# Kernel tuning notes

Measured on AMD Instinct MI355X. Metric: run time of the kernel, lower is better.

Reference implementation:

```python
import jax, jax.numpy as jnp
import numpy as np


def setup_inputs() -> dict:
    key = jax.random.key(0)
    k1, k2, k3, k4 = jax.random.split(key, 4)
    dim, b, q_len, c_len = 1024, 16, 1024, 2048
    q = jax.random.normal(k1, (q_len, b, dim), dtype=jnp.float32)
    c = jax.random.normal(k2, (c_len, b, dim), dtype=jnp.float32)
    # torch nn.Linear weights: [out_features, in_features]
    W_in = jax.random.normal(k3, (dim, dim), dtype=jnp.float32) * (dim ** -0.5)
    W_out = jax.random.normal(k4, (dim, 2 * dim), dtype=jnp.float32) * ((2 * dim) ** -0.5)
    return {"q": q, "c": c, "W_in": W_in, "W_out": W_out}


def reference(q, c, W_in, W_out):
    # q: [q_len, b, dim] -> [b, q_len, dim]; c: [c_len, b, dim] -> [b, c_len, dim]
    qb = jnp.transpose(q, (1, 0, 2))
    cb = jnp.transpose(c, (1, 0, 2))
    qb = jnp.einsum('bqd,ed->bqe', qb, W_in)            # linear_in (no bias)
    score = jnp.einsum('bqd,bkd->bqk', qb, cb)          # unscaled QK^T
    score = jax.nn.softmax(score, axis=-1)              # [b, q_len, c_len]
    ctx = jnp.einsum('bqk,bkd->bqd', score, cb)         # score @ c
    cat = jnp.concatenate([ctx, qb], axis=-1)           # [b, q_len, 2*dim]
    out = jnp.tanh(jnp.einsum('bqf,df->bqd', cat, W_out))
    return (jnp.transpose(out, (1, 0, 2)), score)       # ([q_len,b,dim], [b,q_len,c_len])
```

## Files before the change

kernel.cpp:

```cpp
#include <hip/hip_runtime.h>
#include <hip/hip_bf16.h>
#include <stdint.h>


typedef __bf16 bf16x8 __attribute__((ext_vector_type(8)));
typedef float floatx4 __attribute__((ext_vector_type(4)));

__device__ __forceinline__ unsigned short f2bf_rne(float f) {
  unsigned int u = __float_as_uint(f);
  u += 0x7FFFu + ((u >> 16) & 1u);
  return (unsigned short)(u >> 16);
}
__device__ __forceinline__ float bf2f(unsigned short h) {
  return __uint_as_float(((unsigned int)h) << 16);
}

__device__ __forceinline__ void async_load16(const void* g, void* l) {
  __builtin_amdgcn_global_load_lds(
      (const __attribute__((address_space(1))) void*)g,
      (__attribute__((address_space(3))) void*)l,
      16, 0, 0);
}

__global__ __launch_bounds__(256) void split_kernel(
    const float* __restrict__ x, unsigned short* __restrict__ hi,
    unsigned short* __restrict__ lo, long n4)
{
  long i = (long)blockIdx.x * 256 + threadIdx.x;
  if (i >= n4) return;
  float4 v = ((const float4*)x)[i];
  ushort4 h;
  h.x = f2bf_rne(v.x); h.y = f2bf_rne(v.y);
  h.z = f2bf_rne(v.z); h.w = f2bf_rne(v.w);
  ((ushort4*)hi)[i] = h;
  if (lo) {
    ushort4 l;
    l.x = f2bf_rne(v.x - bf2f(h.x));
    l.y = f2bf_rne(v.y - bf2f(h.y));
    l.z = f2bf_rne(v.z - bf2f(h.z));
    l.w = f2bf_rne(v.w - bf2f(h.w));
    ((ushort4*)lo)[i] = l;
  }
}

__global__ __launch_bounds__(256) void transpose_kernel(
    const float* __restrict__ c, unsigned short* __restrict__ ct)
{
  __shared__ unsigned short t[64 * 68];
  int k0 = blockIdx.x * 64;
  int d0 = blockIdx.y * 64;
  int b  = blockIdx.z;
  int tid = threadIdx.x;
  #pragma unroll
  for (int p4 = 0; p4 < 4; ++p4) {
    int idx = p4 * 256 + tid;
    int kr = idx >> 4;
    int dc = (idx & 15) * 4;
    float4 v = *(const float4*)&c[(long)(k0 + kr) * 16384 + (long)b * 1024 + d0 + dc];
    ushort4 h;
    h.x = f2bf_rne(v.x); h.y = f2bf_rne(v.y);
    h.z = f2bf_rne(v.z); h.w = f2bf_rne(v.w);
    *(ushort4*)&t[kr * 68 + dc] = h;
  }
  __syncthreads();
  #pragma unroll
  for (int p4 = 0; p4 < 4; ++p4) {
    int idx = p4 * 256 + tid;
    int dr = idx >> 4;
    int kc = (idx & 15) * 4;
    ushort4 o;
    o.x = t[(kc + 0) * 68 + dr];
    o.y = t[(kc + 1) * 68 + dr];
    o.z = t[(kc + 2) * 68 + dr];
    o.w = t[(kc + 3) * 68 + dr];
    *(ushort4*)&ct[(long)b * 2097152 + (long)(d0 + dr) * 2048 + k0 + kc] = o;
  }
}

__global__ __launch_bounds__(256) void softmax_kernel(
    float* __restrict__ S, unsigned short* __restrict__ P)
{
  __shared__ float sred[8];
  long row = blockIdx.x;
  float* p = S + row * 2048;
  int tid = threadIdx.x;
  int lane = tid & 63, w = tid >> 6;
  float4 v0 = ((float4*)p)[tid];
  float4 v1 = ((float4*)p)[tid + 256];
  float m = fmaxf(fmaxf(fmaxf(v0.x, v0.y), fmaxf(v0.z, v0.w)),
                  fmaxf(fmaxf(v1.x, v1.y), fmaxf(v1.z, v1.w)));
  #pragma unroll
  for (int off = 32; off; off >>= 1) m = fmaxf(m, __shfl_xor(m, off));
  if (lane == 0) sred[w] = m;
  __syncthreads();
  m = fmaxf(fmaxf(sred[0], sred[1]), fmaxf(sred[2], sred[3]));
  v0.x = __expf(v0.x - m); v0.y = __expf(v0.y - m);
  v0.z = __expf(v0.z - m); v0.w = __expf(v0.w - m);
  v1.x = __expf(v1.x - m); v1.y = __expf(v1.y - m);
  v1.z = __expf(v1.z - m); v1.w = __expf(v1.w - m);
  float s = v0.x + v0.y + v0.z + v0.w + v1.x + v1.y + v1.z + v1.w;
  #pragma unroll
  for (int off = 32; off; off >>= 1) s += __shfl_xor(s, off);
  if (lane == 0) sred[4 + w] = s;
  __syncthreads();
  s = sred[4] + sred[5] + sred[6] + sred[7];
  float inv = 1.0f / s;
  v0.x *= inv; v0.y *= inv; v0.z *= inv; v0.w *= inv;
  v1.x *= inv; v1.y *= inv; v1.z *= inv; v1.w *= inv;
  ((float4*)p)[tid] = v0;
  ((float4*)p)[tid + 256] = v1;
  unsigned short* pp = P + row * 2048;
  ushort4 b0, b1;
  b0.x = f2bf_rne(v0.x); b0.y = f2bf_rne(v0.y);
  b0.z = f2bf_rne(v0.z); b0.w = f2bf_rne(v0.w);
  b1.x = f2bf_rne(v1.x); b1.y = f2bf_rne(v1.y);
  b1.z = f2bf_rne(v1.z); b1.w = f2bf_rne(v1.w);
  ((ushort4*)pp)[tid] = b0;
  ((ushort4*)pp)[tid + 256] = b1;
}

template<int SPLIT, int MODE>
__global__ __launch_bounds__(256, 2) void gemm_kernel(
    const unsigned short* __restrict__ Ah, const unsigned short* __restrict__ Al,
    long sAb, long ldA,
    const unsigned short* __restrict__ Bh, const unsigned short* __restrict__ Bl,
    long sBb, long ldB,
    void* __restrict__ Cp, long sCb, long ldC,
    unsigned short* __restrict__ P1, unsigned short* __restrict__ P2,
    int K, int SM, int SN, int GM)
{
  constexpr int BK  = SPLIT ? 32 : 64;
  constexpr int KB8 = BK / 8;
  constexpr int ISS = (128 * KB8) / 256;
  constexpr int NT  = SPLIT ? 4 : 2;
  __shared__ unsigned short lds[16384];

  const int tid  = threadIdx.x;
  const int lane = tid & 63;
  const int w    = tid >> 6;
  const int wm   = w >> 1;
  const int wn   = w & 1;
  const int bz   = blockIdx.z;

  const int flat = blockIdx.x + gridDim.x * blockIdx.y;
  const int sub  = flat & 7;
  const int g    = flat >> 3;
  const long mt  = (long)(sub % GM) * SM + (g / SN);
  const long nt  = (long)(sub / GM) * SN + (g % SN);
  const long m0  = mt * 128;
  const long n0  = nt * 128;

  const unsigned short* a0 = Ah + bz * sAb + m0 * ldA;
  const unsigned short* a1 = SPLIT ? (Al + bz * sAb + m0 * ldA) : a0;
  const unsigned short* b0 = Bh + bz * sBb + n0 * ldB;
  const unsigned short* b1 = SPLIT ? (Bl + bz * sBb + n0 * ldB) : b0;

  floatx4 acc[4][4] = {};

  for (int kt = 0; kt < K; kt += BK) {
    #pragma unroll
    for (int t = 0; t < NT; ++t) {
      const unsigned short* src;
      long ld;
      int base;
      if (SPLIT) {
        src  = (t == 0) ? a0 : (t == 1) ? a1 : (t == 2) ? b0 : b1;
        ld   = (t < 2) ? ldA : ldB;
        base = t * 4096;
      } else {
        src  = (t == 0) ? a0 : b0;
        ld   = (t == 0) ? ldA : ldB;
        base = t * 8192;
      }
      #pragma unroll
      for (int it = 0; it < ISS; ++it) {
        int s   = it * 256 + tid;
        int row = s / KB8;
        int kb  = (s & (KB8 - 1)) ^ (SPLIT ? ((row >> 1) & 3) : (row & 7));
        const unsigned short* g2 = src + (long)row * ld + kt + kb * 8;
        async_load16(g2, &lds[base + (it * 256 + w * 64) * 8]);
      }
    }
    __syncthreads();

    #pragma unroll
    for (int kk = 0; kk < BK / 32; ++kk) {
      bf16x8 fbh[4], fbl[4];
      #pragma unroll
      for (int j = 0; j < 4; ++j) {
        int r    = wn * 64 + j * 16 + (lane & 15);
        int kb   = (lane >> 4) + kk * 4;
        int slot = r * KB8 + (kb ^ (SPLIT ? ((r >> 1) & 3) : (r & 7)));
        fbh[j] = *(const bf16x8*)&lds[8192 + slot * 8];
        if (SPLIT) fbl[j] = *(const bf16x8*)&lds[12288 + slot * 8];
      }
      #pragma unroll
      for (int i = 0; i < 4; ++i) {
        int r    = wm * 64 + i * 16 + (lane & 15);
        int kb   = (lane >> 4) + kk * 4;
        int slot = r * KB8 + (kb ^ (SPLIT ? ((r >> 1) & 3) : (r & 7)));
        bf16x8 fah = *(const bf16x8*)&lds[slot * 8];
        bf16x8 fal = fah;
        if (SPLIT) fal = *(const bf16x8*)&lds[4096 + slot * 8];
        #pragma unroll
        for (int j = 0; j < 4; ++j) {
          acc[i][j] = __builtin_amdgcn_mfma_f32_16x16x32_bf16(fah, fbh[j], acc[i][j], 0, 0, 0);
          if (SPLIT) {
            acc[i][j] = __builtin_amdgcn_mfma_f32_16x16x32_bf16(fah, fbl[j], acc[i][j], 0, 0, 0);
            acc[i][j] = __builtin_amdgcn_mfma_f32_16x16x32_bf16(fal, fbh[j], acc[i][j], 0, 0, 0);
          }
        }
      }
    }
    __syncthreads();
  }

  #pragma unroll
  for (int i = 0; i < 4; ++i) {
    #pragma unroll
    for (int j = 0; j < 4; ++j) {
      #pragma unroll
      for (int t = 0; t < 4; ++t) {
        long rg = m0 + wm * 64 + i * 16 + (lane >> 4) * 4 + t;
        long cg = n0 + wn * 64 + j * 16 + (lane & 15);
        float v = acc[i][j][t];
        if (MODE == 0) {
          ((float*)Cp)[bz * sCb + rg * ldC + cg] = v;
        } else if (MODE == 1) {
          ((unsigned short*)Cp)[bz * sCb + rg * ldC + cg] = f2bf_rne(v);
        } else if (MODE == 2) {
          long qq = rg & 1023, bb = rg >> 10;
          ((float*)Cp)[(qq * 16 + bb) * 1024 + cg] = tanhf(v);
        } else {
          unsigned short hv = f2bf_rne(v);
          unsigned short lv = f2bf_rne(v - bf2f(hv));
          P1[rg * 1024 + cg] = hv;
          P2[rg * 1024 + cg] = lv;
          long bb = rg & 15, qq = rg >> 4;
          ((unsigned short*)Cp)[(bb * 1024 + qq) * 2048 + 1024 + cg] = hv;
        }
      }
    }
  }
}

extern "C" void kernel_launch(void* const* d_in, const int* in_sizes, int n_in,
                              void* d_out, int out_size, void* d_ws, size_t ws_size,
                              hipStream_t stream)
{
  const float* q    = (const float*)d_in[0];
  const float* c    = (const float*)d_in[1];
  const float* Win  = (const float*)d_in[2];
  const float* Wout = (const float*)d_in[3];

  char* ws = (char*)d_ws;
  const size_t MB = 1024u * 1024u;

  unsigned short* qh  = (unsigned short*)(ws);
  unsigned short* ch  = (unsigned short*)(ws);
  unsigned short* pb  = (unsigned short*)(ws);
  unsigned short* qbh = (unsigned short*)(ws + 64 * MB);
  unsigned short* qbl = (unsigned short*)(ws + 96 * MB);
  unsigned short* ct  = (unsigned short*)(ws + 64 * MB);
  unsigned short* cat = (unsigned short*)(ws + 128 * MB);
  unsigned short* Wh  = (unsigned short*)(ws + 192 * MB);
  unsigned short* Wl  = (unsigned short*)(ws + 194 * MB);
  unsigned short* Wo  = (unsigned short*)(ws + 196 * MB);

  unsigned short* ql  = (unsigned short*)d_out;
  unsigned short* cl  = (unsigned short*)d_out;
  float* out0  = (float*)d_out;
  float* score = (float*)d_out + 16777216;

  split_kernel<<<16384, 256, 0, stream>>>(q,    qh, ql,      4194304L);
  split_kernel<<<1024,  256, 0, stream>>>(Win,  Wh, Wl,      262144L);
  split_kernel<<<2048,  256, 0, stream>>>(Wout, Wo, nullptr, 524288L);

  gemm_kernel<1, 3><<<dim3(128, 8, 1), 256, 0, stream>>>(
      qh, ql, 0L, 1024L, Wh, Wl, 0L, 1024L,
      (void*)cat, 0L, 0L, qbh, qbl, 1024, 32, 4, 4);

  split_kernel<<<32768, 256, 0, stream>>>(c, ch, cl, 8388608L);

  gemm_kernel<1, 0><<<dim3(8, 16, 16), 256, 0, stream>>>(
      qbh, qbl, 1024L, 16384L, ch, cl, 1024L, 16384L,
      (void*)score, 2097152L, 2048L, nullptr, nullptr, 1024, 4, 4, 2);

  transpose_kernel<<<dim3(32, 16, 16), 256, 0, stream>>>(c, ct);
  softmax_kernel<<<16384, 256, 0, stream>>>(score, pb);

  gemm_kernel<0, 1><<<dim3(8, 8, 16), 256, 0, stream>>>(
      pb, nullptr, 2097152L, 2048L, ct, nullptr, 2097152L, 2048L,
      (void*)cat, 2097152L, 2048L, nullptr, nullptr, 2048, 4, 2, 2);

  gemm_kernel<0, 2><<<dim3(128, 8, 1), 256, 0, stream>>>(
      cat, nullptr, 0L, 2048L, Wo, nullptr, 0L, 2048L,
      (void*)out0, 0L, 0L, nullptr, nullptr, 2048, 32, 4, 4);

  (void)in_sizes; (void)n_in; (void)out_size; (void)ws_size;
}
```

Baseline: 964.9 us.

## Rewrite GEMM as 256x256 tile, 512-thread kernel with 4-stage async LDS pipeline

The GEMM kernel moves from 128x128 tiles with 256 threads and a synchronous load-then-compute loop to 256x256 tiles with 512 threads (8 waves, 128x64 per wave). It uses a 4-slot LDS ring buffer with three stages prefetched, explicit vmcnt waits and a single barrier per step. The split-precision (hi/lo) products become three separate virtual k-steps, each issuing one MFMA per fragment pair, and MFMA sections get raised wave priority. This is meant to hide global-to-LDS latency and raise data reuse per loaded byte. In exchange it uses 128KB of LDS and more accumulator registers, which may limit occupancy, and the grids become coarser with fewer blocks per GEMM.

```diff
diff --git a/kernel.cpp b/kernel.cpp
--- a/kernel.cpp
+++ b/kernel.cpp
@@ -120,7 +120,7 @@
 }
 
 template<int SPLIT, int MODE>
-__global__ __launch_bounds__(256, 2) void gemm_kernel(
+__global__ __launch_bounds__(512, 2) void gemm_kernel(
     const unsigned short* __restrict__ Ah, const unsigned short* __restrict__ Al,
     long sAb, long ldA,
     const unsigned short* __restrict__ Bh, const unsigned short* __restrict__ Bl,
@@ -129,17 +129,13 @@
     unsigned short* __restrict__ P1, unsigned short* __restrict__ P2,
     int K, int SM, int SN, int GM)
 {
-  constexpr int BK  = SPLIT ? 32 : 64;
-  constexpr int KB8 = BK / 8;
-  constexpr int ISS = (128 * KB8) / 256;
-  constexpr int NT  = SPLIT ? 4 : 2;
-  __shared__ unsigned short lds[16384];
+  __shared__ __align__(16) unsigned short lds[65536];
 
   const int tid  = threadIdx.x;
   const int lane = tid & 63;
   const int w    = tid >> 6;
-  const int wm   = w >> 1;
-  const int wn   = w & 1;
+  const int wm   = w >> 2;
+  const int wn   = w & 3;
   const int bz   = blockIdx.z;
 
   const int flat = blockIdx.x + gridDim.x * blockIdx.y;
@@ -147,81 +143,92 @@
   const int g    = flat >> 3;
   const long mt  = (long)(sub % GM) * SM + (g / SN);
   const long nt  = (long)(sub / GM) * SN + (g % SN);
-  const long m0  = mt * 128;
-  const long n0  = nt * 128;
+  const long m0  = mt * 256;
+  const long n0  = nt * 256;
 
   const unsigned short* a0 = Ah + bz * sAb + m0 * ldA;
   const unsigned short* a1 = SPLIT ? (Al + bz * sAb + m0 * ldA) : a0;
   const unsigned short* b0 = Bh + bz * sBb + n0 * ldB;
   const unsigned short* b1 = SPLIT ? (Bl + bz * sBb + n0 * ldB) : b0;
 
-  floatx4 acc[4][4] = {};
-
-  for (int kt = 0; kt < K; kt += BK) {
+  const int s0r = tid >> 2,        s1r = (512 + tid) >> 2;
+  const int s0k = (tid & 3) ^ ((s0r >> 1) & 3);
+  const int s1k = ((512 + tid) & 3) ^ ((s1r >> 1) & 3);
+  const long offA0 = (long)s0r * ldA + s0k * 8;
+  const long offA1 = (long)s1r * ldA + s1k * 8;
+  const long offB0 = (long)s0r * ldB + s0k * 8;
+  const long offB1 = (long)s1r * ldB + s1k * 8;
+  const int d0 = w * 512;
+  const int d1 = 4096 + w * 512;
+
+  const int nkt = SPLIT ? 3 * (K / 32) : (K / 32);
+
+  floatx4 acc[8][4] = {};
+
+  auto stage = [&](int vt2) {
+    const int slot = vt2 & 3;
+    const unsigned short* As;
+    const unsigned short* Bs;
+    long ks;
+    if (SPLIT) {
+      int term = vt2 % 3;
+      ks = (long)(vt2 / 3) * 32;
+      As = (term < 2) ? a0 : a1;
+      Bs = (term == 1) ? b1 : b0;
+    } else {
+      As = a0; Bs = b0; ks = (long)vt2 * 32;
+    }
+    const int ab = slot * 8192;
+    const int bb = 32768 + slot * 8192;
+    async_load16(As + offA0 + ks, &lds[ab + d0]);
+    async_load16(As + offA1 + ks, &lds[ab + d1]);
+    async_load16(Bs + offB0 + ks, &lds[bb + d0]);
+    async_load16(Bs + offB1 + ks, &lds[bb + d1]);
+  };
+
+  stage(0); stage(1); stage(2);
+
+  for (int vt = 0; vt < nkt; ++vt) {
+    const int ahead = nkt - 1 - vt;
+    if (ahead >= 2)      asm volatile("s_waitcnt vmcnt(8)" ::: "memory");
+    else if (ahead == 1) asm volatile("s_waitcnt vmcnt(4)" ::: "memory");
+    else                 asm volatile("s_waitcnt vmcnt(0)" ::: "memory");
+    __builtin_amdgcn_s_barrier();
+    __builtin_amdgcn_sched_barrier(0);
+
+    if (vt + 3 < nkt) stage(vt + 3);
+    __builtin_amdgcn_sched_barrier(0);
+
+    const unsigned short* At = &lds[(vt & 3) * 8192];
+    const unsigned short* Bt = &lds[32768 + (vt & 3) * 8192];
+
+    bf16x8 fb[4];
     #pragma unroll
-    for (int t = 0; t < NT; ++t) {
-      const unsigned short* src;
-      long ld;
-      int base;
-      if (SPLIT) {
-        src  = (t == 0) ? a0 : (t == 1) ? a1 : (t == 2) ? b0 : b1;
-        ld   = (t < 2) ? ldA : ldB;
-        base = t * 4096;
-      } else {
-        src  = (t == 0) ? a0 : b0;
-        ld   = (t == 0) ? ldA : ldB;
-        base = t * 8192;
-      }
+    for (int j = 0; j < 4; ++j) {
+      int r    = wn * 64 + j * 16 + (lane & 15);
+      int slot = r * 4 + ((lane >> 4) ^ ((r >> 1) & 3));
+      fb[j] = *(const bf16x8*)&Bt[slot * 8];
+    }
+    __builtin_amdgcn_s_setprio(1);
+    #pragma unroll
+    for (int i = 0; i < 8; ++i) {
+      int r    = wm * 128 + i * 16 + (lane & 15);
+      int slot = r * 4 + ((lane >> 4) ^ ((r >> 1) & 3));
+      bf16x8 fa = *(const bf16x8*)&At[slot * 8];
       #pragma unroll
-      for (int it = 0; it < ISS; ++it) {
-        int s   = it * 256 + tid;
-        int row = s / KB8;
-        int kb  = (s & (KB8 - 1)) ^ (SPLIT ? ((row >> 1) & 3) : (row & 7));
-        const unsigned short* g2 = src + (long)row * ld + kt + kb * 8;
-        async_load16(g2, &lds[base + (it * 256 + w * 64) * 8]);
-      }
+      for (int j = 0; j < 4; ++j)
+        acc[i][j] = __builtin_amdgcn_mfma_f32_16x16x32_bf16(fa, fb[j], acc[i][j], 0, 0, 0);
     }
-    __syncthreads();
-
-    #pragma unroll
-    for (int kk = 0; kk < BK / 32; ++kk) {
-      bf16x8 fbh[4], fbl[4];
-      #pragma unroll
-      for (int j = 0; j < 4; ++j) {
-        int r    = wn * 64 + j * 16 + (lane & 15);
-        int kb   = (lane >> 4) + kk * 4;
-        int slot = r * KB8 + (kb ^ (SPLIT ? ((r >> 1) & 3) : (r & 7)));
-        fbh[j] = *(const bf16x8*)&lds[8192 + slot * 8];
-        if (SPLIT) fbl[j] = *(const bf16x8*)&lds[12288 + slot * 8];
-      }
-      #pragma unroll
-      for (int i = 0; i < 4; ++i) {
-        int r    = wm * 64 + i * 16 + (lane & 15);
-        int kb   = (lane >> 4) + kk * 4;
-        int slot = r * KB8 + (kb ^ (SPLIT ? ((r >> 1) & 3) : (r & 7)));
-        bf16x8 fah = *(const bf16x8*)&lds[slot * 8];
-        bf16x8 fal = fah;
-        if (SPLIT) fal = *(const bf16x8*)&lds[4096 + slot * 8];
-        #pragma unroll
-        for (int j = 0; j < 4; ++j) {
-          acc[i][j] = __builtin_amdgcn_mfma_f32_16x16x32_bf16(fah, fbh[j], acc[i][j], 0, 0, 0);
-          if (SPLIT) {
-            acc[i][j] = __builtin_amdgcn_mfma_f32_16x16x32_bf16(fah, fbl[j], acc[i][j], 0, 0, 0);
-            acc[i][j] = __builtin_amdgcn_mfma_f32_16x16x32_bf16(fal, fbh[j], acc[i][j], 0, 0, 0);
-          }
-        }
-      }
-    }
-    __syncthreads();
-  }
-
-  #pragma unroll
-  for (int i = 0; i < 4; ++i) {
+    __builtin_amdgcn_s_setprio(0);
+  }
+
+  #pragma unroll
+  for (int i = 0; i < 8; ++i) {
     #pragma unroll
     for (int j = 0; j < 4; ++j) {
       #pragma unroll
       for (int t = 0; t < 4; ++t) {
-        long rg = m0 + wm * 64 + i * 16 + (lane >> 4) * 4 + t;
+        long rg = m0 + wm * 128 + i * 16 + (lane >> 4) * 4 + t;
         long cg = n0 + wn * 64 + j * 16 + (lane & 15);
         float v = acc[i][j][t];
         if (MODE == 0) {
@@ -276,26 +283,26 @@
   split_kernel<<<1024,  256, 0, stream>>>(Win,  Wh, Wl,      262144L);
   split_kernel<<<2048,  256, 0, stream>>>(Wout, Wo, nullptr, 524288L);
 
-  gemm_kernel<1, 3><<<dim3(128, 8, 1), 256, 0, stream>>>(
+  gemm_kernel<1, 3><<<dim3(32, 8, 1), 512, 0, stream>>>(
       qh, ql, 0L, 1024L, Wh, Wl, 0L, 1024L,
-      (void*)cat, 0L, 0L, qbh, qbl, 1024, 32, 4, 4);
+      (void*)cat, 0L, 0L, qbh, qbl, 1024, 8, 4, 8);
 
   split_kernel<<<32768, 256, 0, stream>>>(c, ch, cl, 8388608L);
 
-  gemm_kernel<1, 0><<<dim3(8, 16, 16), 256, 0, stream>>>(
+  gemm_kernel<1, 0><<<dim3(4, 8, 16), 512, 0, stream>>>(
       qbh, qbl, 1024L, 16384L, ch, cl, 1024L, 16384L,
-      (void*)score, 2097152L, 2048L, nullptr, nullptr, 1024, 4, 4, 2);
+      (void*)score, 2097152L, 2048L, nullptr, nullptr, 1024, 2, 2, 2);
 
   transpose_kernel<<<dim3(32, 16, 16), 256, 0, stream>>>(c, ct);
   softmax_kernel<<<16384, 256, 0, stream>>>(score, pb);
 
-  gemm_kernel<0, 1><<<dim3(8, 8, 16), 256, 0, stream>>>(
+  gemm_kernel<0, 1><<<dim3(4, 4, 16), 512, 0, stream>>>(
       pb, nullptr, 2097152L, 2048L, ct, nullptr, 2097152L, 2048L,
-      (void*)cat, 2097152L, 2048L, nullptr, nullptr, 2048, 4, 2, 2);
-
-  gemm_kernel<0, 2><<<dim3(128, 8, 1), 256, 0, stream>>>(
+      (void*)cat, 2097152L, 2048L, nullptr, nullptr, 2048, 1, 2, 4);
+
+  gemm_kernel<0, 2><<<dim3(32, 8, 1), 512, 0, stream>>>(
       cat, nullptr, 0L, 2048L, Wo, nullptr, 0L, 2048L,
-      (void*)out0, 0L, 0L, nullptr, nullptr, 2048, 32, 4, 4);
+      (void*)out0, 0L, 0L, nullptr, nullptr, 2048, 8, 4, 8);
 
   (void)in_sizes; (void)n_in; (void)out_size; (void)ws_size;
 }
```

New measurement: 929.3 us. -3.7%, faster.
